# Optimization experiments

Hardware: AMD Instinct MI355X
Metric: run time of the kernel (lower is better)

## Reference

```python
import jax, jax.numpy as jnp
import numpy as np

B, S, I, O = 64, 512, 256, 256


def setup_inputs() -> dict:
    key = jax.random.key(0)
    ks = jax.random.split(key, 7)
    s_i = 1.0 / np.sqrt(I)
    s_o = 1.0 / np.sqrt(O)
    return {
        "x": jax.random.normal(ks[0], (B, S, I), dtype=jnp.float32),
        "h0": jax.random.normal(ks[1], (B, O), dtype=jnp.float32) * 0.1,
        "c0": jax.random.normal(ks[2], (B, O), dtype=jnp.float32) * 0.1,
        # gate order: [f, i, g, o]; Linear convention y = x @ W.T + b
        "Wh": jax.random.normal(ks[3], (4, O, O), dtype=jnp.float32) * s_o,
        "bh": jax.random.normal(ks[4], (4, O), dtype=jnp.float32) * s_o,
        "Wx": jax.random.normal(ks[5], (4, O, I), dtype=jnp.float32) * s_i,
        "bx": jax.random.normal(ks[6], (4, O), dtype=jnp.float32) * s_i,
    }


def reference(x, h0, c0, Wh, bh, Wx, bx):
    # Precompute all input-side gate projections in one big GEMM: [S, B, 4, O]
    xg = jnp.einsum('bsi,goi->sbgo', x, Wx) + bx + bh  # fold both biases here

    def step(carry, xt):
        h, c = carry
        g = jnp.einsum('bo,gpo->bgp', h, Wh) + xt  # [B, 4, O]
        f = jax.nn.sigmoid(g[:, 0])
        i = jax.nn.sigmoid(g[:, 1])
        gt = jnp.tanh(g[:, 2])
        o = jax.nn.sigmoid(g[:, 3])
        c = c * f + i * gt
        h = o * jnp.tanh(c)
        return (h, c), h

    (hT, cT), hs = jax.lax.scan(step, (h0, c0), xg)
    h_seq = jnp.transpose(hs, (1, 0, 2))  # [B, S, O]
    return h_seq, hT, cT
```

## Files before the change

kernel.cpp:

```cpp
#include <hip/hip_runtime.h>


#define SS 512

typedef _Float16 h2 __attribute__((ext_vector_type(2)));

__device__ __forceinline__ h2 bch(unsigned u) { return __builtin_bit_cast(h2, u); }

#if __has_builtin(__builtin_amdgcn_fdot2)
__device__ __forceinline__ float dot2f(h2 a, h2 b, float c) {
  return __builtin_amdgcn_fdot2(a, b, c, false);
}
#else
__device__ __forceinline__ float dot2f(h2 a, h2 b, float c) {
  return c + (float)a[0] * (float)b[0] + (float)a[1] * (float)b[1];
}
#endif

__device__ __forceinline__ float sigm(float x) { return 1.f / (1.f + __expf(-x)); }
__device__ __forceinline__ float tanh_f(float x) {
  float e = __expf(-2.f * fabsf(x));
  float r = (1.f - e) / (1.f + e);
  return copysignf(r, x);
}

__global__ __launch_bounds__(256) void xg_gemm(
    const float* __restrict__ X, const float* __restrict__ W,
    const float* __restrict__ bx, const float* __restrict__ bh,
    float* __restrict__ out)
{
  __shared__ float As[64][68];
  __shared__ float Bs[64][68];
  const int bm = blockIdx.x >> 4;
  const int bn = blockIdx.x & 15;
  const int tid = threadIdx.x;
  const int tn = tid & 15, tm = tid >> 4;
  const int row0 = bm * 64, col0 = bn * 64;
  float acc[4][4] = {};

  for (int k0 = 0; k0 < 256; k0 += 64) {
#pragma unroll
    for (int i = 0; i < 4; i++) {
      const int m = (tid >> 4) + i * 16;
      const int k = (tid & 15) * 4;
      float4 av = *(const float4*)&X[(size_t)(row0 + m) * 256 + k0 + k];
      *(float4*)&As[m][k] = av;
      float4 wv = *(const float4*)&W[(size_t)(col0 + m) * 256 + k0 + k];
      Bs[k + 0][m] = wv.x; Bs[k + 1][m] = wv.y;
      Bs[k + 2][m] = wv.z; Bs[k + 3][m] = wv.w;
    }
    __syncthreads();
#pragma unroll 8
    for (int kk = 0; kk < 64; kk++) {
      const float a0 = As[tm * 4 + 0][kk];
      const float a1 = As[tm * 4 + 1][kk];
      const float a2 = As[tm * 4 + 2][kk];
      const float a3 = As[tm * 4 + 3][kk];
      const float4 bv = *(const float4*)&Bs[kk][tn * 4];
      acc[0][0] = fmaf(a0, bv.x, acc[0][0]); acc[0][1] = fmaf(a0, bv.y, acc[0][1]);
      acc[0][2] = fmaf(a0, bv.z, acc[0][2]); acc[0][3] = fmaf(a0, bv.w, acc[0][3]);
      acc[1][0] = fmaf(a1, bv.x, acc[1][0]); acc[1][1] = fmaf(a1, bv.y, acc[1][1]);
      acc[1][2] = fmaf(a1, bv.z, acc[1][2]); acc[1][3] = fmaf(a1, bv.w, acc[1][3]);
      acc[2][0] = fmaf(a2, bv.x, acc[2][0]); acc[2][1] = fmaf(a2, bv.y, acc[2][1]);
      acc[2][2] = fmaf(a2, bv.z, acc[2][2]); acc[2][3] = fmaf(a2, bv.w, acc[2][3]);
      acc[3][0] = fmaf(a3, bv.x, acc[3][0]); acc[3][1] = fmaf(a3, bv.y, acc[3][1]);
      acc[3][2] = fmaf(a3, bv.z, acc[3][2]); acc[3][3] = fmaf(a3, bv.w, acc[3][3]);
    }
    __syncthreads();
  }

  float bias[4];
#pragma unroll
  for (int j = 0; j < 4; j++) {
    const int col = col0 + tn * 4 + j;
    bias[j] = bx[col] + bh[col];
  }
#pragma unroll
  for (int i = 0; i < 4; i++) {
    float4 o4;
    o4.x = acc[i][0] + bias[0]; o4.y = acc[i][1] + bias[1];
    o4.z = acc[i][2] + bias[2]; o4.w = acc[i][3] + bias[3];
    *(float4*)&out[(size_t)(row0 + tm * 4 + i) * 1024 + col0 + tn * 4] = o4;
  }
}

__global__ __launch_bounds__(512, 2) void lstm_scan2(
    const float* __restrict__ xg,
    const float* __restrict__ Wh,
    const float* __restrict__ h0,
    const float* __restrict__ c0,
    float* __restrict__ out)
{
  __shared__ __align__(16) _Float16 wl[2 * 8 * 512 * 8];
  __shared__ __align__(16) _Float16 h_sh[256];
  __shared__ float io_i[256];
  __shared__ float io_o[256];

  const int tid = threadIdx.x;
  const int b = blockIdx.x;

  const float* r0 = Wh + (size_t)tid * 256;
  const float* r1 = Wh + (size_t)(tid + 512) * 256;

  h2 w0[96], w1[96];
#pragma unroll
  for (int j = 0; j < 96; ++j) {
    float2 a = *(const float2*)&r0[2 * j];
    float2 c = *(const float2*)&r1[2 * j];
    h2 wa; wa[0] = (_Float16)a.x; wa[1] = (_Float16)a.y; w0[j] = wa;
    h2 wc; wc[0] = (_Float16)c.x; wc[1] = (_Float16)c.y; w1[j] = wc;
  }
#pragma unroll
  for (int c = 0; c < 8; ++c) {
#pragma unroll
    for (int e = 0; e < 8; ++e) {
      wl[((size_t)(c)*512 + tid) * 8 + e]     = (_Float16)r0[192 + c * 8 + e];
      wl[((size_t)(8 + c)*512 + tid) * 8 + e] = (_Float16)r1[192 + c * 8 + e];
    }
  }
  if (tid < 256) h_sh[tid] = (_Float16)h0[(size_t)b * 256 + tid];
  float cr = (tid < 256) ? c0[(size_t)b * 256 + tid] : 0.f;
  __syncthreads();

  const float* xr = xg + (size_t)b * SS * 1024;
  float* hs = out + (size_t)b * SS * 256;

  for (int t = 0; t < SS; ++t) {
    const float xg0 = xr[(size_t)t * 1024 + tid];
    const float xg1 = xr[(size_t)t * 1024 + tid + 512];

    float A0 = 0.f, B0 = 0.f, A1 = 0.f, B1 = 0.f;
#pragma unroll
    for (int c2 = 0; c2 < 12; ++c2) {
      uint4 ha = *(const uint4*)&h_sh[c2 * 16];
      uint4 hb = *(const uint4*)&h_sh[c2 * 16 + 8];
      const int j = c2 * 8;
      A0 = dot2f(w0[j + 0], bch(ha.x), A0); A1 = dot2f(w1[j + 0], bch(ha.x), A1);
      B0 = dot2f(w0[j + 1], bch(ha.y), B0); B1 = dot2f(w1[j + 1], bch(ha.y), B1);
      A0 = dot2f(w0[j + 2], bch(ha.z), A0); A1 = dot2f(w1[j + 2], bch(ha.z), A1);
      B0 = dot2f(w0[j + 3], bch(ha.w), B0); B1 = dot2f(w1[j + 3], bch(ha.w), B1);
      A0 = dot2f(w0[j + 4], bch(hb.x), A0); A1 = dot2f(w1[j + 4], bch(hb.x), A1);
      B0 = dot2f(w0[j + 5], bch(hb.y), B0); B1 = dot2f(w1[j + 5], bch(hb.y), B1);
      A0 = dot2f(w0[j + 6], bch(hb.z), A0); A1 = dot2f(w1[j + 6], bch(hb.z), A1);
      B0 = dot2f(w0[j + 7], bch(hb.w), B0); B1 = dot2f(w1[j + 7], bch(hb.w), B1);
    }
#pragma unroll
    for (int c = 0; c < 8; ++c) {
      uint4 hw = *(const uint4*)&h_sh[192 + c * 8];
      uint4 wa = *(const uint4*)&wl[((size_t)(c)*512 + tid) * 8];
      uint4 wb = *(const uint4*)&wl[((size_t)(8 + c)*512 + tid) * 8];
      A0 = dot2f(bch(wa.x), bch(hw.x), A0); A1 = dot2f(bch(wb.x), bch(hw.x), A1);
      B0 = dot2f(bch(wa.y), bch(hw.y), B0); B1 = dot2f(bch(wb.y), bch(hw.y), B1);
      A0 = dot2f(bch(wa.z), bch(hw.z), A0); A1 = dot2f(bch(wb.z), bch(hw.z), A1);
      B0 = dot2f(bch(wa.w), bch(hw.w), B0); B1 = dot2f(bch(wb.w), bch(hw.w), B1);
    }
    const float y0 = A0 + B0 + xg0;
    const float y1 = A1 + B1 + xg1;

    float u0 = 0.f, u1 = 0.f;
    if (tid < 256) {
      u0 = sigm(y0);
      u1 = tanh_f(y1);
    } else {
      io_i[tid - 256] = sigm(y0);
      io_o[tid - 256] = sigm(y1);
    }
    __syncthreads();

    if (tid < 256) {
      cr = cr * u0 + io_i[tid] * u1;
      const float h = io_o[tid] * tanh_f(cr);
      hs[(size_t)t * 256 + tid] = h;
      h_sh[tid] = (_Float16)h;
      if (t == SS - 1) {
        out[8388608 + (size_t)b * 256 + tid] = h;
        out[8404992 + (size_t)b * 256 + tid] = cr;
      }
    }
    __syncthreads();
  }
}

extern "C" void kernel_launch(void* const* d_in, const int* in_sizes, int n_in,
                              void* d_out, int out_size, void* d_ws, size_t ws_size,
                              hipStream_t stream) {
  const float* x  = (const float*)d_in[0];
  const float* h0 = (const float*)d_in[1];
  const float* c0 = (const float*)d_in[2];
  const float* Wh = (const float*)d_in[3];
  const float* bh = (const float*)d_in[4];
  const float* Wx = (const float*)d_in[5];
  const float* bx = (const float*)d_in[6];
  float* out = (float*)d_out;

  float* xg = (float*)d_ws;

  xg_gemm<<<dim3(8192), dim3(256), 0, stream>>>(x, Wx, bx, bh, xg);
  lstm_scan2<<<dim3(64), dim3(512), 0, stream>>>(xg, Wh, h0, c0, out);
}
```

Baseline: 1.239 ms.

## Give each thread all four gates of one hidden unit in LSTM scan

The recurrent scan now runs 256 threads per block, and each thread computes all four gate pre-activations for one hidden unit. This removes the shared-memory exchange of the i/o gates and one of the barriers' dependent phases. Weights for the first 224 inputs sit in registers (448 half2 values) with the rest in LDS, and the next step's xg values are prefetched one step ahead. The trade-off is half as many threads per block, a much larger register footprint that risks spilling, and longer serial dot-product chains per thread.

Result: slower. 1.913 ms (+54.5%).

```diff
diff --git a/kernel.cpp b/kernel.cpp
--- a/kernel.cpp
+++ b/kernel.cpp
@@ -2,6 +2,7 @@
 
 
 #define SS 512
+#define KR 224
 
 typedef _Float16 h2 __attribute__((ext_vector_type(2)));
 
@@ -84,101 +85,103 @@
   }
 }
 
-__global__ __launch_bounds__(512, 2) void lstm_scan2(
+__global__ __launch_bounds__(256, 1) void lstm_scan3(
     const float* __restrict__ xg,
     const float* __restrict__ Wh,
     const float* __restrict__ h0,
     const float* __restrict__ c0,
     float* __restrict__ out)
 {
-  __shared__ __align__(16) _Float16 wl[2 * 8 * 512 * 8];
+  __shared__ __align__(16) _Float16 wl[4 * 4 * 256 * 8];
   __shared__ __align__(16) _Float16 h_sh[256];
-  __shared__ float io_i[256];
-  __shared__ float io_o[256];
 
   const int tid = threadIdx.x;
   const int b = blockIdx.x;
 
-  const float* r0 = Wh + (size_t)tid * 256;
-  const float* r1 = Wh + (size_t)(tid + 512) * 256;
-
-  h2 w0[96], w1[96];
-#pragma unroll
-  for (int j = 0; j < 96; ++j) {
-    float2 a = *(const float2*)&r0[2 * j];
-    float2 c = *(const float2*)&r1[2 * j];
-    h2 wa; wa[0] = (_Float16)a.x; wa[1] = (_Float16)a.y; w0[j] = wa;
-    h2 wc; wc[0] = (_Float16)c.x; wc[1] = (_Float16)c.y; w1[j] = wc;
-  }
-#pragma unroll
-  for (int c = 0; c < 8; ++c) {
-#pragma unroll
-    for (int e = 0; e < 8; ++e) {
-      wl[((size_t)(c)*512 + tid) * 8 + e]     = (_Float16)r0[192 + c * 8 + e];
-      wl[((size_t)(8 + c)*512 + tid) * 8 + e] = (_Float16)r1[192 + c * 8 + e];
-    }
-  }
-  if (tid < 256) h_sh[tid] = (_Float16)h0[(size_t)b * 256 + tid];
-  float cr = (tid < 256) ? c0[(size_t)b * 256 + tid] : 0.f;
+  h2 w[4][KR / 2];
+#pragma unroll
+  for (int g = 0; g < 4; ++g) {
+    const float* r = Wh + ((size_t)(g * 256) + tid) * 256;
+#pragma unroll
+    for (int j = 0; j < KR / 2; ++j) {
+      float2 a = *(const float2*)&r[2 * j];
+      h2 v; v[0] = (_Float16)a.x; v[1] = (_Float16)a.y;
+      w[g][j] = v;
+    }
+#pragma unroll
+    for (int c = 0; c < 4; ++c)
+#pragma unroll
+      for (int e = 0; e < 8; ++e)
+        wl[(((g * 4 + c) * 256) + tid) * 8 + e] = (_Float16)r[KR + c * 8 + e];
+  }
+  h_sh[tid] = (_Float16)h0[(size_t)b * 256 + tid];
+  float cr = c0[(size_t)b * 256 + tid];
   __syncthreads();
 
-  const float* xr = xg + (size_t)b * SS * 1024;
+  const float* xr = xg + (size_t)b * SS * 1024 + tid;
   float* hs = out + (size_t)b * SS * 256;
 
+  float x0 = xr[0], x1 = xr[256], x2 = xr[512], x3 = xr[768];
+  float hlast = 0.f;
+
   for (int t = 0; t < SS; ++t) {
-    const float xg0 = xr[(size_t)t * 1024 + tid];
-    const float xg1 = xr[(size_t)t * 1024 + tid + 512];
-
-    float A0 = 0.f, B0 = 0.f, A1 = 0.f, B1 = 0.f;
-#pragma unroll
-    for (int c2 = 0; c2 < 12; ++c2) {
+    float nx0 = 0.f, nx1 = 0.f, nx2 = 0.f, nx3 = 0.f;
+    if (t + 1 < SS) {
+      const float* xn = xr + (size_t)(t + 1) * 1024;
+      nx0 = xn[0]; nx1 = xn[256]; nx2 = xn[512]; nx3 = xn[768];
+    }
+
+    float a0 = x0, a1 = x1, a2 = x2, a3 = x3;
+#pragma unroll
+    for (int c2 = 0; c2 < KR / 16; ++c2) {
       uint4 ha = *(const uint4*)&h_sh[c2 * 16];
       uint4 hb = *(const uint4*)&h_sh[c2 * 16 + 8];
+      unsigned hv[8] = {ha.x, ha.y, ha.z, ha.w, hb.x, hb.y, hb.z, hb.w};
       const int j = c2 * 8;
-      A0 = dot2f(w0[j + 0], bch(ha.x), A0); A1 = dot2f(w1[j + 0], bch(ha.x), A1);
-      B0 = dot2f(w0[j + 1], bch(ha.y), B0); B1 = dot2f(w1[j + 1], bch(ha.y), B1);
-      A0 = dot2f(w0[j + 2], bch(ha.z), A0); A1 = dot2f(w1[j + 2], bch(ha.z), A1);
-      B0 = dot2f(w0[j + 3], bch(ha.w), B0); B1 = dot2f(w1[j + 3], bch(ha.w), B1);
-      A0 = dot2f(w0[j + 4], bch(hb.x), A0); A1 = dot2f(w1[j + 4], bch(hb.x), A1);
-      B0 = dot2f(w0[j + 5], bch(hb.y), B0); B1 = dot2f(w1[j + 5], bch(hb.y), B1);
-      A0 = dot2f(w0[j + 6], bch(hb.z), A0); A1 = dot2f(w1[j + 6], bch(hb.z), A1);
-      B0 = dot2f(w0[j + 7], bch(hb.w), B0); B1 = dot2f(w1[j + 7], bch(hb.w), B1);
-    }
-#pragma unroll
-    for (int c = 0; c < 8; ++c) {
-      uint4 hw = *(const uint4*)&h_sh[192 + c * 8];
-      uint4 wa = *(const uint4*)&wl[((size_t)(c)*512 + tid) * 8];
-      uint4 wb = *(const uint4*)&wl[((size_t)(8 + c)*512 + tid) * 8];
-      A0 = dot2f(bch(wa.x), bch(hw.x), A0); A1 = dot2f(bch(wb.x), bch(hw.x), A1);
-      B0 = dot2f(bch(wa.y), bch(hw.y), B0); B1 = dot2f(bch(wb.y), bch(hw.y), B1);
-      A0 = dot2f(bch(wa.z), bch(hw.z), A0); A1 = dot2f(bch(wb.z), bch(hw.z), A1);
-      B0 = dot2f(bch(wa.w), bch(hw.w), B0); B1 = dot2f(bch(wb.w), bch(hw.w), B1);
-    }
-    const float y0 = A0 + B0 + xg0;
-    const float y1 = A1 + B1 + xg1;
-
-    float u0 = 0.f, u1 = 0.f;
-    if (tid < 256) {
-      u0 = sigm(y0);
-      u1 = tanh_f(y1);
-    } else {
-      io_i[tid - 256] = sigm(y0);
-      io_o[tid - 256] = sigm(y1);
-    }
-    __syncthreads();
-
-    if (tid < 256) {
-      cr = cr * u0 + io_i[tid] * u1;
-      const float h = io_o[tid] * tanh_f(cr);
-      hs[(size_t)t * 256 + tid] = h;
-      h_sh[tid] = (_Float16)h;
-      if (t == SS - 1) {
-        out[8388608 + (size_t)b * 256 + tid] = h;
-        out[8404992 + (size_t)b * 256 + tid] = cr;
+#pragma unroll
+      for (int u = 0; u < 8; ++u) {
+        const h2 hh = bch(hv[u]);
+        a0 = dot2f(w[0][j + u], hh, a0);
+        a1 = dot2f(w[1][j + u], hh, a1);
+        a2 = dot2f(w[2][j + u], hh, a2);
+        a3 = dot2f(w[3][j + u], hh, a3);
       }
     }
-    __syncthreads();
-  }
+#pragma unroll
+    for (int c = 0; c < 4; ++c) {
+      uint4 hw = *(const uint4*)&h_sh[KR + c * 8];
+      unsigned hv2[4] = {hw.x, hw.y, hw.z, hw.w};
+      uint4 w0 = *(const uint4*)&wl[(((0 * 4 + c) * 256) + tid) * 8];
+      uint4 w1 = *(const uint4*)&wl[(((1 * 4 + c) * 256) + tid) * 8];
+      uint4 w2 = *(const uint4*)&wl[(((2 * 4 + c) * 256) + tid) * 8];
+      uint4 w3 = *(const uint4*)&wl[(((3 * 4 + c) * 256) + tid) * 8];
+      a0 = dot2f(bch(w0.x), bch(hv2[0]), a0); a0 = dot2f(bch(w0.y), bch(hv2[1]), a0);
+      a0 = dot2f(bch(w0.z), bch(hv2[2]), a0); a0 = dot2f(bch(w0.w), bch(hv2[3]), a0);
+      a1 = dot2f(bch(w1.x), bch(hv2[0]), a1); a1 = dot2f(bch(w1.y), bch(hv2[1]), a1);
+      a1 = dot2f(bch(w1.z), bch(hv2[2]), a1); a1 = dot2f(bch(w1.w), bch(hv2[3]), a1);
+      a2 = dot2f(bch(w2.x), bch(hv2[0]), a2); a2 = dot2f(bch(w2.y), bch(hv2[1]), a2);
+      a2 = dot2f(bch(w2.z), bch(hv2[2]), a2); a2 = dot2f(bch(w2.w), bch(hv2[3]), a2);
+      a3 = dot2f(bch(w3.x), bch(hv2[0]), a3); a3 = dot2f(bch(w3.y), bch(hv2[1]), a3);
+      a3 = dot2f(bch(w3.z), bch(hv2[2]), a3); a3 = dot2f(bch(w3.w), bch(hv2[3]), a3);
+    }
+
+    const float fg = sigm(a0);
+    const float ig = sigm(a1);
+    const float gt = tanh_f(a2);
+    const float og = sigm(a3);
+    cr = cr * fg + ig * gt;
+    const float h = og * tanh_f(cr);
+    hlast = h;
+
+    __syncthreads();
+    h_sh[tid] = (_Float16)h;
+    hs[(size_t)t * 256 + tid] = h;
+    x0 = nx0; x1 = nx1; x2 = nx2; x3 = nx3;
+    __syncthreads();
+  }
+
+  out[8388608 + (size_t)b * 256 + tid] = hlast;
+  out[8404992 + (size_t)b * 256 + tid] = cr;
 }
 
 extern "C" void kernel_launch(void* const* d_in, const int* in_sizes, int n_in,
@@ -196,5 +199,5 @@
   float* xg = (float*)d_ws;
 
   xg_gemm<<<dim3(8192), dim3(256), 0, stream>>>(x, Wx, bx, bh, xg);
-  lstm_scan2<<<dim3(64), dim3(512), 0, stream>>>(xg, Wh, h0, c0, out);
-}
+  lstm_scan3<<<dim3(64), dim3(256), 0, stream>>>(xg, Wh, h0, c0, out);
+}
```

## Use MFMA for recurrent matvec in LSTM scan with double-buffered hidden state

Applied to the files above, without the earlier changes.

Replaces the per-thread fdot2 recurrent matvec with 16x16x32 f16 MFMA instructions. Weight fragments stay in registers, and a tail slice lives in LDS. The hidden state is broadcast as the B operand, so only column 0 of each output tile is used, which wastes most of the MFMA work but drops the per-thread dot loops. The change also double-buffers h in LDS, regroups gate activations so 256 threads handle all four gates, and defers the global h store by one step to overlap it with the next step's compute.

New measurement: 1.323 ms. 1.07x slower.

```diff
diff --git a/kernel.cpp b/kernel.cpp
--- a/kernel.cpp
+++ b/kernel.cpp
@@ -3,19 +3,8 @@
 
 #define SS 512
 
-typedef _Float16 h2 __attribute__((ext_vector_type(2)));
-
-__device__ __forceinline__ h2 bch(unsigned u) { return __builtin_bit_cast(h2, u); }
-
-#if __has_builtin(__builtin_amdgcn_fdot2)
-__device__ __forceinline__ float dot2f(h2 a, h2 b, float c) {
-  return __builtin_amdgcn_fdot2(a, b, c, false);
-}
-#else
-__device__ __forceinline__ float dot2f(h2 a, h2 b, float c) {
-  return c + (float)a[0] * (float)b[0] + (float)a[1] * (float)b[1];
-}
-#endif
+typedef _Float16 v8h __attribute__((ext_vector_type(8)));
+typedef float vf4 __attribute__((ext_vector_type(4)));
 
 __device__ __forceinline__ float sigm(float x) { return 1.f / (1.f + __expf(-x)); }
 __device__ __forceinline__ float tanh_f(float x) {
@@ -84,100 +73,121 @@
   }
 }
 
-__global__ __launch_bounds__(512, 2) void lstm_scan2(
+__global__ __launch_bounds__(512) void lstm_scan5(
     const float* __restrict__ xg,
     const float* __restrict__ Wh,
     const float* __restrict__ h0,
     const float* __restrict__ c0,
     float* __restrict__ out)
 {
-  __shared__ __align__(16) _Float16 wl[2 * 8 * 512 * 8];
-  __shared__ __align__(16) _Float16 h_sh[256];
-  __shared__ float io_i[256];
-  __shared__ float io_o[256];
-
-  const int tid = threadIdx.x;
-  const int b = blockIdx.x;
-
-  const float* r0 = Wh + (size_t)tid * 256;
-  const float* r1 = Wh + (size_t)(tid + 512) * 256;
-
-  h2 w0[96], w1[96];
-#pragma unroll
-  for (int j = 0; j < 96; ++j) {
-    float2 a = *(const float2*)&r0[2 * j];
-    float2 c = *(const float2*)&r1[2 * j];
-    h2 wa; wa[0] = (_Float16)a.x; wa[1] = (_Float16)a.y; w0[j] = wa;
-    h2 wc; wc[0] = (_Float16)c.x; wc[1] = (_Float16)c.y; w1[j] = wc;
-  }
-#pragma unroll
-  for (int c = 0; c < 8; ++c) {
-#pragma unroll
-    for (int e = 0; e < 8; ++e) {
-      wl[((size_t)(c)*512 + tid) * 8 + e]     = (_Float16)r0[192 + c * 8 + e];
-      wl[((size_t)(8 + c)*512 + tid) * 8 + e] = (_Float16)r1[192 + c * 8 + e];
-    }
-  }
-  if (tid < 256) h_sh[tid] = (_Float16)h0[(size_t)b * 256 + tid];
-  float cr = (tid < 256) ? c0[(size_t)b * 256 + tid] : 0.f;
+  __shared__ __align__(16) _Float16 wtail[8 * 8 * 2 * 64 * 8];
+  __shared__ __align__(16) _Float16 hbuf[2][256];
+  __shared__ __align__(16) float ylds[4][256];
+
+  const int tid  = threadIdx.x;
+  const int b    = blockIdx.x;
+  const int w    = tid >> 6;
+  const int lane = tid & 63;
+  const int q    = lane >> 4;
+  const int l15  = lane & 15;
+
+  v8h A[8][6];
+#pragma unroll
+  for (int j = 0; j < 8; ++j) {
+    const int g = j >> 1, i = j & 1;
+    const float* rp = Wh + (size_t)(g * 256 + w * 32 + i * 16 + l15) * 256 + q * 8;
+#pragma unroll
+    for (int kf = 0; kf < 6; ++kf) {
+      float4 lo = *(const float4*)(rp + kf * 32);
+      float4 hi = *(const float4*)(rp + kf * 32 + 4);
+      v8h a;
+      a[0] = (_Float16)lo.x; a[1] = (_Float16)lo.y;
+      a[2] = (_Float16)lo.z; a[3] = (_Float16)lo.w;
+      a[4] = (_Float16)hi.x; a[5] = (_Float16)hi.y;
+      a[6] = (_Float16)hi.z; a[7] = (_Float16)hi.w;
+      A[j][kf] = a;
+    }
+#pragma unroll
+    for (int kfi = 0; kfi < 2; ++kfi) {
+      float4 lo = *(const float4*)(rp + 192 + kfi * 32);
+      float4 hi = *(const float4*)(rp + 192 + kfi * 32 + 4);
+      _Float16* dst = &wtail[((((w * 8 + j) * 2) + kfi) * 64 + lane) * 8];
+      dst[0] = (_Float16)lo.x; dst[1] = (_Float16)lo.y;
+      dst[2] = (_Float16)lo.z; dst[3] = (_Float16)lo.w;
+      dst[4] = (_Float16)hi.x; dst[5] = (_Float16)hi.y;
+      dst[6] = (_Float16)hi.z; dst[7] = (_Float16)hi.w;
+    }
+  }
+
+  if (tid < 256) hbuf[0][tid] = (_Float16)h0[(size_t)b * 256 + tid];
+  float c = (tid < 256) ? c0[(size_t)b * 256 + tid] : 0.f;
   __syncthreads();
 
-  const float* xr = xg + (size_t)b * SS * 1024;
+  const float* xb = xg + (size_t)b * SS * 1024;
   float* hs = out + (size_t)b * SS * 256;
+  float hprev = 0.f;
 
   for (int t = 0; t < SS; ++t) {
-    const float xg0 = xr[(size_t)t * 1024 + tid];
-    const float xg1 = xr[(size_t)t * 1024 + tid + 512];
-
-    float A0 = 0.f, B0 = 0.f, A1 = 0.f, B1 = 0.f;
-#pragma unroll
-    for (int c2 = 0; c2 < 12; ++c2) {
-      uint4 ha = *(const uint4*)&h_sh[c2 * 16];
-      uint4 hb = *(const uint4*)&h_sh[c2 * 16 + 8];
-      const int j = c2 * 8;
-      A0 = dot2f(w0[j + 0], bch(ha.x), A0); A1 = dot2f(w1[j + 0], bch(ha.x), A1);
-      B0 = dot2f(w0[j + 1], bch(ha.y), B0); B1 = dot2f(w1[j + 1], bch(ha.y), B1);
-      A0 = dot2f(w0[j + 2], bch(ha.z), A0); A1 = dot2f(w1[j + 2], bch(ha.z), A1);
-      B0 = dot2f(w0[j + 3], bch(ha.w), B0); B1 = dot2f(w1[j + 3], bch(ha.w), B1);
-      A0 = dot2f(w0[j + 4], bch(hb.x), A0); A1 = dot2f(w1[j + 4], bch(hb.x), A1);
-      B0 = dot2f(w0[j + 5], bch(hb.y), B0); B1 = dot2f(w1[j + 5], bch(hb.y), B1);
-      A0 = dot2f(w0[j + 6], bch(hb.z), A0); A1 = dot2f(w1[j + 6], bch(hb.z), A1);
-      B0 = dot2f(w0[j + 7], bch(hb.w), B0); B1 = dot2f(w1[j + 7], bch(hb.w), B1);
-    }
-#pragma unroll
-    for (int c = 0; c < 8; ++c) {
-      uint4 hw = *(const uint4*)&h_sh[192 + c * 8];
-      uint4 wa = *(const uint4*)&wl[((size_t)(c)*512 + tid) * 8];
-      uint4 wb = *(const uint4*)&wl[((size_t)(8 + c)*512 + tid) * 8];
-      A0 = dot2f(bch(wa.x), bch(hw.x), A0); A1 = dot2f(bch(wb.x), bch(hw.x), A1);
-      B0 = dot2f(bch(wa.y), bch(hw.y), B0); B1 = dot2f(bch(wb.y), bch(hw.y), B1);
-      A0 = dot2f(bch(wa.z), bch(hw.z), A0); A1 = dot2f(bch(wb.z), bch(hw.z), A1);
-      B0 = dot2f(bch(wa.w), bch(hw.w), B0); B1 = dot2f(bch(wb.w), bch(hw.w), B1);
-    }
-    const float y0 = A0 + B0 + xg0;
-    const float y1 = A1 + B1 + xg1;
-
-    float u0 = 0.f, u1 = 0.f;
+    const int par = t & 1;
+
+    float xc0 = 0.f, xc1 = 0.f, xc2 = 0.f, xc3 = 0.f;
     if (tid < 256) {
-      u0 = sigm(y0);
-      u1 = tanh_f(y1);
-    } else {
-      io_i[tid - 256] = sigm(y0);
-      io_o[tid - 256] = sigm(y1);
+      if (t > 0) hs[(size_t)(t - 1) * 256 + tid] = hprev;
+      const float* xp = xb + (size_t)t * 1024 + tid;
+      xc0 = xp[0]; xc1 = xp[256]; xc2 = xp[512]; xc3 = xp[768];
+    }
+
+    vf4 D[8];
+#pragma unroll
+    for (int j = 0; j < 8; ++j) { vf4 z = {0.f, 0.f, 0.f, 0.f}; D[j] = z; }
+
+#pragma unroll
+    for (int kf = 0; kf < 6; ++kf) {
+      v8h Bf = *(const v8h*)&hbuf[par][kf * 32 + q * 8];
+#pragma unroll
+      for (int j = 0; j < 8; ++j)
+        D[j] = __builtin_amdgcn_mfma_f32_16x16x32_f16(A[j][kf], Bf, D[j], 0, 0, 0);
+    }
+#pragma unroll
+    for (int kfi = 0; kfi < 2; ++kfi) {
+      v8h Bf = *(const v8h*)&hbuf[par][(6 + kfi) * 32 + q * 8];
+#pragma unroll
+      for (int j = 0; j < 8; ++j) {
+        v8h wt = *(const v8h*)&wtail[((((w * 8 + j) * 2) + kfi) * 64 + lane) * 8];
+        D[j] = __builtin_amdgcn_mfma_f32_16x16x32_f16(wt, Bf, D[j], 0, 0, 0);
+      }
+    }
+
+    if (l15 == 0) {
+#pragma unroll
+      for (int j = 0; j < 8; ++j) {
+        const int g = j >> 1, i = j & 1;
+        *(vf4*)&ylds[g][w * 32 + i * 16 + q * 4] = D[j];
+      }
     }
     __syncthreads();
 
     if (tid < 256) {
-      cr = cr * u0 + io_i[tid] * u1;
-      const float h = io_o[tid] * tanh_f(cr);
-      hs[(size_t)t * 256 + tid] = h;
-      h_sh[tid] = (_Float16)h;
-      if (t == SS - 1) {
-        out[8388608 + (size_t)b * 256 + tid] = h;
-        out[8404992 + (size_t)b * 256 + tid] = cr;
-      }
-    }
-    __syncthreads();
+      const float y0 = ylds[0][tid] + xc0;
+      const float y1 = ylds[1][tid] + xc1;
+      const float y2 = ylds[2][tid] + xc2;
+      const float y3 = ylds[3][tid] + xc3;
+      const float fg = sigm(y0);
+      const float ig = sigm(y1);
+      const float gt = tanh_f(y2);
+      const float og = sigm(y3);
+      c = c * fg + ig * gt;
+      const float h = og * tanh_f(c);
+      hprev = h;
+      hbuf[par ^ 1][tid] = (_Float16)h;
+    }
+    __syncthreads();
+  }
+
+  if (tid < 256) {
+    hs[(size_t)(SS - 1) * 256 + tid] = hprev;
+    out[8388608 + (size_t)b * 256 + tid] = hprev;
+    out[8404992 + (size_t)b * 256 + tid] = c;
   }
 }
 
@@ -196,5 +206,5 @@
   float* xg = (float*)d_ws;
 
   xg_gemm<<<dim3(8192), dim3(256), 0, stream>>>(x, Wx, bx, bh, xg);
-  lstm_scan2<<<dim3(64), dim3(512), 0, stream>>>(xg, Wh, h0, c0, out);
-}
+  lstm_scan5<<<dim3(64), dim3(512), 0, stream>>>(xg, Wh, h0, c0, out);
+}
```
